# Performance work log

Measured on AMD Instinct MI355X. Metric: run time of the kernel, lower is better.

Reference implementation:

```python
import jax, jax.numpy as jnp
import numpy as np

EMBED_DIMS = 256
NUM_GROUPS = 8
NUM_LEVELS = 4
NUM_CAMS = 6
NUM_LEARNABLE_PTS = 6
FIX_SCALE = np.array([[0,0,0],[0.45,0,0],[-0.45,0,0],[0,0.45,0],[0,-0.45,0],[0,0,0.45],[0,0,-0.45]], dtype=np.float32)
NUM_PTS = len(FIX_SCALE) + NUM_LEARNABLE_PTS  # 13
GROUP_DIMS = EMBED_DIMS // NUM_GROUPS


def safe_sigmoid(x):
    return jax.nn.sigmoid(jnp.clip(x, -9.21, 9.21))


def get_rotation_matrix(q):
    # q: [..., 4] quaternion (w, x, y, z), normalized first (GaussianFormer convention)
    q = q / jnp.linalg.norm(q, axis=-1, keepdims=True)
    w, x, y, z = q[..., 0], q[..., 1], q[..., 2], q[..., 3]
    R = jnp.stack([
        jnp.stack([1 - 2 * (y * y + z * z), 2 * (x * y - w * z), 2 * (x * z + w * y)], axis=-1),
        jnp.stack([2 * (x * y + w * z), 1 - 2 * (x * x + z * z), 2 * (y * z - w * x)], axis=-1),
        jnp.stack([2 * (x * z - w * y), 2 * (y * z + w * x), 1 - 2 * (x * x + y * y)], axis=-1),
    ], axis=-2)
    return R  # [..., 3, 3]


def key_points_generator(anchor, instance_feature, W_learn, b_learn):
    bs, num_anchor = anchor.shape[:2]
    fix_scale = jnp.asarray(FIX_SCALE, anchor.dtype)  # [7, 3]
    scale = jnp.broadcast_to(fix_scale[None, None], (bs, num_anchor, fix_scale.shape[0], 3))
    learnable = safe_sigmoid((instance_feature @ W_learn + b_learn)
                             .reshape(bs, num_anchor, NUM_LEARNABLE_PTS, 3)) - 0.5
    scale = jnp.concatenate([scale, learnable], axis=-2)         # [bs, na, P, 3]
    gs_scales = anchor[..., None, 3:6]                           # [bs, na, 1, 3]
    key_points = scale * gs_scales                               # [bs, na, P, 3]
    rot_T = jnp.swapaxes(get_rotation_matrix(anchor[..., 6:10]), -1, -2)  # [bs, na, 3, 3]
    key_points = jnp.einsum('bnij,bnpj->bnpi', rot_T, key_points)
    return key_points + anchor[..., None, :3]                    # [bs, na, P, 3]


def project_points(key_points, projection_mat, image_wh):
    # key_points [bs, na, P, 3], projection_mat [bs, cams, 4, 4]
    ones = jnp.ones_like(key_points[..., :1])
    pts4 = jnp.concatenate([key_points, ones], axis=-1)          # [bs, na, P, 4]
    p2d = jnp.einsum('bcij,bnpj->bcnpi', projection_mat, pts4)   # [bs, cams, na, P, 4]
    p2d = p2d[..., :2] / jnp.maximum(p2d[..., 2:3], 1e-5)
    p2d = p2d / image_wh[:, :, None, None]
    return jnp.clip(p2d, 0.0, 0.9999)                            # [bs, cams, na, P, 2]


def bilinear_sample(feat, pts):
    # feat [bs, cams, C, H, W], pts [bs, P, cams, 2] normalized to [0,1]
    bs, cams, C, H, W = feat.shape
    x = pts[..., 0] * W - 0.5
    y = pts[..., 1] * H - 0.5
    x0 = jnp.floor(x); y0 = jnp.floor(y)
    wx = x - x0; wy = y - y0
    x0i = x0.astype(jnp.int32); y0i = y0.astype(jnp.int32)
    feat_f = jnp.transpose(feat, (0, 1, 3, 4, 2)).reshape(bs, cams, H * W, C)
    b_idx = jnp.arange(bs)[:, None, None]
    c_idx = jnp.arange(cams)[None, None, :]

    def gather(yy, xx):
        valid = (yy >= 0) & (yy < H) & (xx >= 0) & (xx < W)
        yc = jnp.clip(yy, 0, H - 1)
        xc = jnp.clip(xx, 0, W - 1)
        v = feat_f[b_idx, c_idx, yc * W + xc]                    # [bs, P, cams, C]
        return v * valid[..., None].astype(v.dtype)

    v00 = gather(y0i, x0i)
    v01 = gather(y0i, x0i + 1)
    v10 = gather(y0i + 1, x0i)
    v11 = gather(y0i + 1, x0i + 1)
    wx = wx[..., None]; wy = wy[..., None]
    return (v00 * (1 - wx) * (1 - wy) + v01 * wx * (1 - wy)
            + v10 * (1 - wx) * wy + v11 * wx * wy)               # [bs, P, cams, C]


def deformable_aggregate(feature_maps, points_2d, weights):
    # points_2d [bs, P, cams, 2]; weights [bs, P, cams, levels, groups]
    bs, P = points_2d.shape[:2]
    out = jnp.zeros((bs, P, NUM_GROUPS, GROUP_DIMS), points_2d.dtype)
    for l, feat in enumerate(feature_maps):
        samp = bilinear_sample(feat, points_2d)                  # [bs, P, cams, C]
        samp = samp.reshape(bs, P, feat.shape[1], NUM_GROUPS, GROUP_DIMS)
        out = out + jnp.einsum('bpcgd,bpcg->bpgd', samp, weights[:, :, :, l, :])
    return out.reshape(bs, P, EMBED_DIMS)


def _forward(pts3d, instance_feature, anchor, feat0, feat1, feat2, feat3,
             projection_mat, image_wh, W_learn, b_learn, W_wts, b_wts, W_out, b_out):
    bs, num_anchor = instance_feature.shape[:2]
    key_points = key_points_generator(anchor, instance_feature, W_learn, b_learn)
    # softmax weights over cams*levels*pts jointly, per group
    w = (instance_feature @ W_wts + b_wts).reshape(bs, num_anchor, -1, NUM_GROUPS)
    w = jax.nn.softmax(w, axis=-2)
    w = w.reshape(bs, num_anchor, NUM_CAMS, NUM_LEVELS, NUM_PTS, NUM_GROUPS)
    w = jnp.transpose(w, (0, 1, 4, 2, 3, 5)).reshape(bs, num_anchor * NUM_PTS, NUM_CAMS, NUM_LEVELS, NUM_GROUPS)
    p2d = project_points(key_points, projection_mat, image_wh)   # [bs, cams, na, P, 2]
    p2d = jnp.transpose(p2d, (0, 2, 3, 1, 4)).reshape(bs, num_anchor * NUM_PTS, NUM_CAMS, 2)
    feats = deformable_aggregate([feat0, feat1, feat2, feat3], p2d, w)
    feats = feats.reshape(bs, num_anchor, NUM_PTS, EMBED_DIMS).sum(axis=2)
    output = feats @ W_out + b_out
    return output + instance_feature


def setup_inputs() -> dict:
    key = jax.random.key(0)
    ks = jax.random.split(key, 16)
    bs, na = 1, 4096
    shapes = [(bs, 6, 256, 64, 176), (bs, 6, 256, 32, 88), (bs, 6, 256, 16, 44), (bs, 6, 256, 8, 22)]
    inp = {
        'pts3d': jax.random.normal(ks[0], (100000, 3), jnp.float32),
        'instance_feature': jax.random.normal(ks[1], (bs, na, EMBED_DIMS), jnp.float32),
        'anchor': jax.random.normal(ks[2], (bs, na, 11), jnp.float32),
        'feat0': jax.random.normal(ks[3], shapes[0], jnp.float32),
        'feat1': jax.random.normal(ks[4], shapes[1], jnp.float32),
        'feat2': jax.random.normal(ks[5], shapes[2], jnp.float32),
        'feat3': jax.random.normal(ks[6], shapes[3], jnp.float32),
        'projection_mat': jax.random.normal(ks[7], (bs, NUM_CAMS, 4, 4), jnp.float32),
        'image_wh': jnp.broadcast_to(jnp.array([704.0, 256.0], jnp.float32), (bs, NUM_CAMS, 2)),
        'W_learn': jax.random.normal(ks[8], (EMBED_DIMS, NUM_LEARNABLE_PTS * 3), jnp.float32) * 0.02,
        'b_learn': jnp.zeros((NUM_LEARNABLE_PTS * 3,), jnp.float32),
        'W_wts': jax.random.normal(ks[9], (EMBED_DIMS, NUM_GROUPS * NUM_CAMS * NUM_LEVELS * NUM_PTS), jnp.float32) * 0.02,
        'b_wts': jnp.zeros((NUM_GROUPS * NUM_CAMS * NUM_LEVELS * NUM_PTS,), jnp.float32),
        'W_out': jax.random.normal(ks[10], (EMBED_DIMS, EMBED_DIMS), jnp.float32) * 0.02,
        'b_out': jnp.zeros((EMBED_DIMS,), jnp.float32),
    }
    return inp


def reference(pts3d, instance_feature, anchor, feat0, feat1, feat2, feat3,
              projection_mat, image_wh, W_learn, b_learn, W_wts, b_wts, W_out, b_out):
    return _forward(pts3d, instance_feature, anchor, feat0, feat1, feat2, feat3,
                    projection_mat, image_wh, W_learn, b_learn, W_wts, b_wts, W_out, b_out)
```

## Files before the change

kernel.cpp:

```cpp
#include <hip/hip_runtime.h>
#include <math.h>


#define FT_L0 0
#define FT_L1 17301504
#define FT_L2 21626880
#define FT_L3 22708224
#define WS_LOGB 5744640
#define WS_FEATB 10856448
#define WS_LEARN 11380736
#define WS_AB 11454464
#define WS_BB 11978752
#define WS_WOB 12306432

typedef float v2f __attribute__((ext_vector_type(2)));
typedef __attribute__((ext_vector_type(8))) short bf16x8;
typedef __attribute__((ext_vector_type(4))) float f32x4;

__device__ const float FIXS[7][3] = {
    {0.f, 0.f, 0.f},  {0.45f, 0.f, 0.f}, {-0.45f, 0.f, 0.f}, {0.f, 0.45f, 0.f},
    {0.f, -0.45f, 0.f}, {0.f, 0.f, 0.45f}, {0.f, 0.f, -0.45f}};

__device__ __forceinline__ unsigned int f2bf(float f) {
  unsigned int u = __float_as_uint(f);
  u += 0x7fffu + ((u >> 16) & 1u);
  return u >> 16;
}
__device__ __forceinline__ float bf2f(unsigned short u) {
  return __uint_as_float(((unsigned int)u) << 16);
}

__global__ __launch_bounds__(256) void k_transpose_all(
    const float* __restrict__ f0, const float* __restrict__ f1,
    const float* __restrict__ f2, const float* __restrict__ f3,
    unsigned char* __restrict__ featF) {
  const int bx = blockIdx.x;
  const float* src;
  unsigned char* dst;
  int H, W, xt;
  if (bx < 6)       { src = f0; dst = featF + FT_L0; H = 64; W = 176; xt = bx * 32; }
  else if (bx < 9)  { src = f1; dst = featF + FT_L1; H = 32; W = 88;  xt = (bx - 6) * 32; }
  else if (bx < 11) { src = f2; dst = featF + FT_L2; H = 16; W = 44;  xt = (bx - 9) * 32; }
  else              { src = f3; dst = featF + FT_L3; H = 8;  W = 22;  xt = 0; }
  const int y = blockIdx.y;
  if (y >= H) return;
  __shared__ float tile[32][33];
  const int tid = threadIdx.x;
  const int i = tid & 31;
  const int j = tid >> 5;
  const int c = blockIdx.z >> 3;
  const int cht = (blockIdx.z & 7) * 32;
#pragma unroll
  for (int jj = j; jj < 32; jj += 8) {
    int x = xt + i;
    float v = 0.f;
    if (x < W) v = src[((c * 256 + cht + jj) * H + y) * W + x];
    tile[jj][i] = v;
  }
  __syncthreads();
  const int q = tid & 7;
  const int xw = tid >> 3;
  const int x = xt + xw;
  if (x < W) {
    const float v0 = tile[q * 4 + 0][xw];
    const float v1 = tile[q * 4 + 1][xw];
    const float v2 = tile[q * 4 + 2][xw];
    const float v3 = tile[q * 4 + 3][xw];
    int pk = __builtin_amdgcn_cvt_pk_fp8_f32(v0, v1, 0, false);
    pk = __builtin_amdgcn_cvt_pk_fp8_f32(v2, v3, pk, true);
    *(unsigned int*)(dst + (((c * H + y) * W + x) * 256) + cht + q * 4) =
        (unsigned int)pk;
  }
}

__global__ __launch_bounds__(256) void k_prep_pack(
    const float* __restrict__ iw, const float* __restrict__ Ww,
    const float* __restrict__ Wl, const float* __restrict__ Wo,
    unsigned short* __restrict__ Ab, unsigned short* __restrict__ Bb,
    unsigned short* __restrict__ Wob) {
  __shared__ unsigned short tile[32][33];
  const int tid = threadIdx.x;
  const int bx = blockIdx.x;
  if (bx < 1024) {
    const int i = bx * 256 + tid;
    const float4 v = ((const float4*)iw)[i];
    uint2 o;
    o.x = f2bf(v.x) | (f2bf(v.y) << 16);
    o.y = f2bf(v.z) | (f2bf(v.w) << 16);
    ((uint2*)Ab)[i] = o;
    return;
  }
  const int i = tid & 31;
  const int r = tid >> 5;
  if (bx < 1664) {
    const int idx = bx - 1024;
    const int j0 = (idx % 80) * 32;
    const int k0 = (idx / 80) * 32;
#pragma unroll
    for (int rr = r; rr < 32; rr += 8) {
      const int k = k0 + rr, j = j0 + i;
      float v = 0.f;
      if (j < 2496) v = Ww[k * 2496 + j];
      else if (j < 2514) v = Wl[k * 18 + (j - 2496)];
      tile[rr][i] = (unsigned short)f2bf(v);
    }
    __syncthreads();
#pragma unroll
    for (int rr = r; rr < 32; rr += 8)
      Bb[(j0 + rr) * 256 + k0 + i] = tile[i][rr];
  } else {
    const int idx = bx - 1664;
    const int j0 = (idx & 7) * 32;
    const int k0 = (idx >> 3) * 32;
#pragma unroll
    for (int rr = r; rr < 32; rr += 8)
      tile[rr][i] = (unsigned short)f2bf(Wo[(k0 + rr) * 256 + j0 + i]);
    __syncthreads();
#pragma unroll
    for (int rr = r; rr < 32; rr += 8)
      Wob[(j0 + rr) * 256 + k0 + i] = tile[i][rr];
  }
}

__global__ __launch_bounds__(256) void k_wts_mfma(
    const unsigned short* __restrict__ Ab, const unsigned short* __restrict__ Bb,
    const float* __restrict__ b_wts, const float* __restrict__ b_learn,
    unsigned short* __restrict__ logitsB, float* __restrict__ learn) {
  const int tid = threadIdx.x;
  const int w = tid >> 6, lane = tid & 63;
  const int ml = lane & 15, q = lane >> 4;
  const int n0 = blockIdx.x * 64;
  const int m0 = blockIdx.y * 64;
  f32x4 acc[4] = {{0.f, 0.f, 0.f, 0.f}, {0.f, 0.f, 0.f, 0.f},
                  {0.f, 0.f, 0.f, 0.f}, {0.f, 0.f, 0.f, 0.f}};
  const unsigned short* Ap = Ab + (m0 + w * 16 + ml) * 256 + q * 8;
  const unsigned short* Bp = Bb + (n0 + ml) * 256 + q * 8;
#pragma unroll
  for (int kk = 0; kk < 8; ++kk) {
    const bf16x8 a = *(const bf16x8*)(Ap + kk * 32);
#pragma unroll
    for (int nt = 0; nt < 4; ++nt) {
      const bf16x8 b = *(const bf16x8*)(Bp + nt * 16 * 256 + kk * 32);
      acc[nt] = __builtin_amdgcn_mfma_f32_16x16x32_bf16(a, b, acc[nt], 0, 0, 0);
    }
  }
  const int rowb = m0 + w * 16 + q * 4;
#pragma unroll
  for (int nt = 0; nt < 4; ++nt) {
    const int col = n0 + nt * 16 + ml;
    if (col < 2496) {
      const float b = b_wts[col];
#pragma unroll
      for (int r = 0; r < 4; ++r)
        logitsB[(rowb + r) * 2496 + col] = (unsigned short)f2bf(acc[nt][r] + b);
    } else if (col < 2514) {
      const float b = b_learn[col - 2496];
#pragma unroll
      for (int r = 0; r < 4; ++r) {
        float v = fminf(fmaxf(acc[nt][r] + b, -9.21f), 9.21f);
        learn[(rowb + r) * 18 + (col - 2496)] = 1.f / (1.f + expf(-v)) - 0.5f;
      }
    }
  }
}

__global__ __launch_bounds__(256, 6) void k_sample(
    const float* __restrict__ anchor, const unsigned short* __restrict__ logitsB,
    const float* __restrict__ learn_g, const unsigned char* __restrict__ featF,
    const float* __restrict__ proj, const float* __restrict__ wh,
    unsigned short* __restrict__ featsB) {
  const int n = blockIdx.x;
  const int tid = threadIdx.x;
  const int lane = tid & 63;
  const int wave = tid >> 6;
  __shared__ unsigned short s_w[8 * 328];
  __shared__ float s_p2d[78][2];
  __shared__ float s_learn[18];
  __shared__ int4 s_off[320];
  __shared__ float4 s_wt[320];
  __shared__ float s_red[4][256];

  for (int i = tid; i < 2496; i += 256) {
    const int s = i >> 3, g = i & 7;
    const int c = s / 52;
    const int r = s - c * 52;
    const int l = r / 13;
    const int p = r - l * 13;
    s_w[g * 328 + (p * 6 + c) * 4 + l] = logitsB[n * 2496 + i];
  }
  if (tid < 64) s_w[(tid >> 3) * 328 + 312 + (tid & 7)] = 0;
  if (tid < 18) s_learn[tid] = learn_g[n * 18 + tid];
  __syncthreads();

#pragma unroll
  for (int gg = 0; gg < 2; ++gg) {
    unsigned short* row = &s_w[(wave * 2 + gg) * 328];
    float l[5];
    float mx = -1e30f;
#pragma unroll
    for (int i = 0; i < 5; ++i) {
      const int s = lane + i * 64;
      l[i] = (s < 312) ? bf2f(row[s]) : -1e30f;
      mx = fmaxf(mx, l[i]);
    }
    for (int off = 32; off; off >>= 1) mx = fmaxf(mx, __shfl_xor(mx, off));
    float sum = 0.f;
#pragma unroll
    for (int i = 0; i < 5; ++i) {
      l[i] = __expf(l[i] - mx);
      sum += l[i];
    }
    for (int off = 32; off; off >>= 1) sum += __shfl_xor(sum, off);
    const float inv = 1.f / sum;
#pragma unroll
    for (int i = 0; i < 5; ++i) {
      const int s = lane + i * 64;
      if (s < 312) row[s] = (unsigned short)f2bf(l[i] * inv);
    }
  }

  if (tid < 78) {
    const int p = tid / 6, c = tid % 6;
    const float* an = anchor + n * 11;
    float qw = an[6], qx = an[7], qy = an[8], qz = an[9];
    const float qinv = 1.f / sqrtf(qw * qw + qx * qx + qy * qy + qz * qz);
    qw *= qinv; qx *= qinv; qy *= qinv; qz *= qinv;
    const float R00 = 1.f - 2.f * (qy * qy + qz * qz), R01 = 2.f * (qx * qy - qw * qz), R02 = 2.f * (qx * qz + qw * qy);
    const float R10 = 2.f * (qx * qy + qw * qz), R11 = 1.f - 2.f * (qx * qx + qz * qz), R12 = 2.f * (qy * qz - qw * qx);
    const float R20 = 2.f * (qx * qz - qw * qy), R21 = 2.f * (qy * qz + qw * qx), R22 = 1.f - 2.f * (qx * qx + qy * qy);
    float s0, s1, s2;
    if (p < 7) {
      s0 = FIXS[p][0]; s1 = FIXS[p][1]; s2 = FIXS[p][2];
    } else {
      const int b = (p - 7) * 3;
      s0 = s_learn[b]; s1 = s_learn[b + 1]; s2 = s_learn[b + 2];
    }
    const float vx = s0 * an[3], vy = s1 * an[4], vz = s2 * an[5];
    const float kx = R00 * vx + R10 * vy + R20 * vz + an[0];
    const float ky = R01 * vx + R11 * vy + R21 * vz + an[1];
    const float kz = R02 * vx + R12 * vy + R22 * vz + an[2];
    const float* P = proj + c * 16;
    const float h0 = P[0] * kx + P[1] * ky + P[2] * kz + P[3];
    const float h1 = P[4] * kx + P[5] * ky + P[6] * kz + P[7];
    const float h2 = P[8] * kx + P[9] * ky + P[10] * kz + P[11];
    const float zz = fmaxf(h2, 1e-5f);
    float px = h0 / zz / wh[c * 2 + 0];
    float py = h1 / zz / wh[c * 2 + 1];
    px = fminf(fmaxf(px, 0.f), 0.9999f);
    py = fminf(fmaxf(py, 0.f), 0.9999f);
    s_p2d[tid][0] = px;
    s_p2d[tid][1] = py;
  }
  __syncthreads();

  {
    constexpr int LBB[4] = {FT_L0, FT_L1, FT_L2, FT_L3};
    constexpr int CSB[4] = {2883584, 720896, 180224, 45056};
    for (int t = tid; t < 320; t += 256) {
      const int pc = t >> 2, l = t & 3;
      if (pc >= 78) {
        s_off[t] = make_int4(0, 0, 0, 0);
        s_wt[t] = make_float4(0.f, 0.f, 0.f, 0.f);
        continue;
      }
      const int c = pc % 6;
      const int H = 64 >> l, W = 176 >> l;
      const float fx = s_p2d[pc][0] * (float)W - 0.5f;
      const float fy = s_p2d[pc][1] * (float)H - 0.5f;
      const float x0f = floorf(fx), y0f = floorf(fy);
      const float wx = fx - x0f, wy = fy - y0f;
      const int x0 = (int)x0f, y0 = (int)y0f;
      const float mx0 = (x0 >= 0) ? 1.f : 0.f;
      const float mx1 = (x0 + 1 < W) ? 1.f : 0.f;
      const float my0 = (y0 >= 0) ? 1.f : 0.f;
      const float my1 = (y0 + 1 < H) ? 1.f : 0.f;
      const int cx0 = max(x0, 0), cx1 = min(x0 + 1, W - 1);
      const int cy0 = max(y0, 0), cy1 = min(y0 + 1, H - 1);
      const int base = LBB[l] + c * CSB[l];
      int4 o;
      o.x = base + (cy0 * W + cx0) * 256;
      o.y = base + (cy0 * W + cx1) * 256;
      o.z = base + (cy1 * W + cx0) * 256;
      o.w = base + (cy1 * W + cx1) * 256;
      s_off[t] = o;
      float4 w4;
      w4.x = (1.f - wx) * (1.f - wy) * mx0 * my0;
      w4.y = wx * (1.f - wy) * mx1 * my0;
      w4.z = (1.f - wx) * wy * mx0 * my1;
      w4.w = wx * wy * mx1 * my1;
      s_wt[t] = w4;
    }
  }
  __syncthreads();

  const int q = lane >> 4;
  const int ql = lane & 15;
  const int chb = ql * 16;
  const int g = ql >> 1;
  v2f acc[8];
#pragma unroll
  for (int k = 0; k < 8; ++k) acc[k] = (v2f){0.f, 0.f};
  const unsigned char* fb = featF;
  const unsigned short* wrow = &s_w[g * 328];
  const int pcb = wave * 4 + q;
#pragma unroll
  for (int it = 0; it < 5; ++it) {
    const int pc = pcb + it * 16;
    const int t0 = pc * 4;
    const uint2 wq = *(const uint2*)&wrow[t0];
    float wgl[4];
    wgl[0] = __uint_as_float(wq.x << 16);
    wgl[1] = __uint_as_float(wq.x & 0xffff0000u);
    wgl[2] = __uint_as_float(wq.y << 16);
    wgl[3] = __uint_as_float(wq.y & 0xffff0000u);
#pragma unroll
    for (int l4 = 0; l4 < 4; ++l4) {
      const int t = t0 + l4;
      const int4 o = s_off[t];
      const float4 bw = s_wt[t];
      const float wg = wgl[l4];
      const uint4 u0 = *(const uint4*)(fb + (o.x + chb));
      const uint4 u1 = *(const uint4*)(fb + (o.y + chb));
      const uint4 u2 = *(const uint4*)(fb + (o.z + chb));
      const uint4 u3 = *(const uint4*)(fb + (o.w + chb));
      const float s0 = bw.x * wg, s1 = bw.y * wg, s2 = bw.z * wg, s3 = bw.w * wg;
      const v2f w0 = {s0, s0}, w1 = {s1, s1}, w2 = {s2, s2}, w3 = {s3, s3};
      acc[0] += __builtin_amdgcn_cvt_pk_f32_fp8((int)u0.x, false) * w0;
      acc[1] += __builtin_amdgcn_cvt_pk_f32_fp8((int)u0.x, true)  * w0;
      acc[2] += __builtin_amdgcn_cvt_pk_f32_fp8((int)u0.y, false) * w0;
      acc[3] += __builtin_amdgcn_cvt_pk_f32_fp8((int)u0.y, true)  * w0;
      acc[4] += __builtin_amdgcn_cvt_pk_f32_fp8((int)u0.z, false) * w0;
      acc[5] += __builtin_amdgcn_cvt_pk_f32_fp8((int)u0.z, true)  * w0;
      acc[6] += __builtin_amdgcn_cvt_pk_f32_fp8((int)u0.w, false) * w0;
      acc[7] += __builtin_amdgcn_cvt_pk_f32_fp8((int)u0.w, true)  * w0;
      acc[0] += __builtin_amdgcn_cvt_pk_f32_fp8((int)u1.x, false) * w1;
      acc[1] += __builtin_amdgcn_cvt_pk_f32_fp8((int)u1.x, true)  * w1;
      acc[2] += __builtin_amdgcn_cvt_pk_f32_fp8((int)u1.y, false) * w1;
      acc[3] += __builtin_amdgcn_cvt_pk_f32_fp8((int)u1.y, true)  * w1;
      acc[4] += __builtin_amdgcn_cvt_pk_f32_fp8((int)u1.z, false) * w1;
      acc[5] += __builtin_amdgcn_cvt_pk_f32_fp8((int)u1.z, true)  * w1;
      acc[6] += __builtin_amdgcn_cvt_pk_f32_fp8((int)u1.w, false) * w1;
      acc[7] += __builtin_amdgcn_cvt_pk_f32_fp8((int)u1.w, true)  * w1;
      acc[0] += __builtin_amdgcn_cvt_pk_f32_fp8((int)u2.x, false) * w2;
      acc[1] += __builtin_amdgcn_cvt_pk_f32_fp8((int)u2.x, true)  * w2;
      acc[2] += __builtin_amdgcn_cvt_pk_f32_fp8((int)u2.y, false) * w2;
      acc[3] += __builtin_amdgcn_cvt_pk_f32_fp8((int)u2.y, true)  * w2;
      acc[4] += __builtin_amdgcn_cvt_pk_f32_fp8((int)u2.z, false) * w2;
      acc[5] += __builtin_amdgcn_cvt_pk_f32_fp8((int)u2.z, true)  * w2;
      acc[6] += __builtin_amdgcn_cvt_pk_f32_fp8((int)u2.w, false) * w2;
      acc[7] += __builtin_amdgcn_cvt_pk_f32_fp8((int)u2.w, true)  * w2;
      acc[0] += __builtin_amdgcn_cvt_pk_f32_fp8((int)u3.x, false) * w3;
      acc[1] += __builtin_amdgcn_cvt_pk_f32_fp8((int)u3.x, true)  * w3;
      acc[2] += __builtin_amdgcn_cvt_pk_f32_fp8((int)u3.y, false) * w3;
      acc[3] += __builtin_amdgcn_cvt_pk_f32_fp8((int)u3.y, true)  * w3;
      acc[4] += __builtin_amdgcn_cvt_pk_f32_fp8((int)u3.z, false) * w3;
      acc[5] += __builtin_amdgcn_cvt_pk_f32_fp8((int)u3.z, true)  * w3;
      acc[6] += __builtin_amdgcn_cvt_pk_f32_fp8((int)u3.w, false) * w3;
      acc[7] += __builtin_amdgcn_cvt_pk_f32_fp8((int)u3.w, true)  * w3;
    }
  }
#pragma unroll
  for (int k = 0; k < 8; ++k) {
    v2f b;
    b.x = __shfl_xor(acc[k].x, 16);
    b.y = __shfl_xor(acc[k].y, 16);
    acc[k] += b;
    b.x = __shfl_xor(acc[k].x, 32);
    b.y = __shfl_xor(acc[k].y, 32);
    acc[k] += b;
  }
  if (lane < 16) {
    float* dst = &s_red[wave][ql * 16];
    *(float4*)(dst + 0)  = make_float4(acc[0].x, acc[0].y, acc[1].x, acc[1].y);
    *(float4*)(dst + 4)  = make_float4(acc[2].x, acc[2].y, acc[3].x, acc[3].y);
    *(float4*)(dst + 8)  = make_float4(acc[4].x, acc[4].y, acc[5].x, acc[5].y);
    *(float4*)(dst + 12) = make_float4(acc[6].x, acc[6].y, acc[7].x, acc[7].y);
  }
  __syncthreads();
  {
    const float sum = s_red[0][tid] + s_red[1][tid] + s_red[2][tid] + s_red[3][tid];
    featsB[n * 256 + tid] = (unsigned short)f2bf(sum);
  }
}

__global__ __launch_bounds__(256) void k_out_mfma(
    const unsigned short* __restrict__ Ab, const unsigned short* __restrict__ Bb,
    const float* __restrict__ bias, const float* __restrict__ resid,
    float* __restrict__ out) {
  const int tid = threadIdx.x;
  const int w = tid >> 6, lane = tid & 63;
  const int ml = lane & 15, q = lane >> 4;
  const int n0 = blockIdx.x * 64;
  const int m0 = blockIdx.y * 64;
  f32x4 acc[4] = {{0.f, 0.f, 0.f, 0.f}, {0.f, 0.f, 0.f, 0.f},
                  {0.f, 0.f, 0.f, 0.f}, {0.f, 0.f, 0.f, 0.f}};
  const unsigned short* Ap = Ab + (m0 + w * 16 + ml) * 256 + q * 8;
  const unsigned short* Bp = Bb + (n0 + ml) * 256 + q * 8;
#pragma unroll
  for (int kk = 0; kk < 8; ++kk) {
    const bf16x8 a = *(const bf16x8*)(Ap + kk * 32);
#pragma unroll
    for (int nt = 0; nt < 4; ++nt) {
      const bf16x8 b = *(const bf16x8*)(Bp + nt * 16 * 256 + kk * 32);
      acc[nt] = __builtin_amdgcn_mfma_f32_16x16x32_bf16(a, b, acc[nt], 0, 0, 0);
    }
  }
  const int rowb = m0 + w * 16 + q * 4;
#pragma unroll
  for (int nt = 0; nt < 4; ++nt) {
    const int col = n0 + nt * 16 + ml;
    const float b = bias[col];
#pragma unroll
    for (int r = 0; r < 4; ++r) {
      const int row = rowb + r;
      out[row * 256 + col] = acc[nt][r] + b + resid[row * 256 + col];
    }
  }
}

extern "C" void kernel_launch(void* const* d_in, const int* in_sizes, int n_in,
                              void* d_out, int out_size, void* d_ws, size_t ws_size,
                              hipStream_t stream) {
  (void)in_sizes; (void)n_in; (void)out_size; (void)ws_size;
  const float* iw      = (const float*)d_in[1];
  const float* anchor  = (const float*)d_in[2];
  const float* f0      = (const float*)d_in[3];
  const float* f1      = (const float*)d_in[4];
  const float* f2      = (const float*)d_in[5];
  const float* f3      = (const float*)d_in[6];
  const float* proj    = (const float*)d_in[7];
  const float* wh      = (const float*)d_in[8];
  const float* W_learn = (const float*)d_in[9];
  const float* b_learn = (const float*)d_in[10];
  const float* W_wts   = (const float*)d_in[11];
  const float* b_wts   = (const float*)d_in[12];
  const float* W_out   = (const float*)d_in[13];
  const float* b_out   = (const float*)d_in[14];
  float* out = (float*)d_out;
  float* ws = (float*)d_ws;
  unsigned char*  featF   = (unsigned char*)ws;
  unsigned short* logitsB = (unsigned short*)(ws + WS_LOGB);
  unsigned short* featsB  = (unsigned short*)(ws + WS_FEATB);
  float*          learn   = ws + WS_LEARN;
  unsigned short* Ab      = (unsigned short*)(ws + WS_AB);
  unsigned short* Bb      = (unsigned short*)(ws + WS_BB);
  unsigned short* Wob     = (unsigned short*)(ws + WS_WOB);

  k_transpose_all<<<dim3(12, 64, 48), 256, 0, stream>>>(f0, f1, f2, f3, featF);
  k_prep_pack<<<1728, 256, 0, stream>>>(iw, W_wts, W_learn, W_out, Ab, Bb, Wob);
  k_wts_mfma<<<dim3(40, 64), 256, 0, stream>>>(Ab, Bb, b_wts, b_learn, logitsB, learn);
  k_sample<<<4096, 256, 0, stream>>>(anchor, logitsB, learn, featF, proj, wh, featsB);
  k_out_mfma<<<dim3(4, 64), 256, 0, stream>>>(featsB, Wob, b_out, iw, out);
}
```

Baseline: 303.9 us.

## Permute weight columns and fuse exp into GEMM epilogue to simplify softmax load

The weight matrix columns are reordered during packing so the GEMM writes logits already in the per-group padded layout that the sampling kernel uses. The exp is applied in the GEMM epilogue, so the sampling kernel loads with a plain contiguous copy and only sums and normalizes. The max-subtraction is dropped, which relies on the logits staying small enough not to overflow, and the sampling kernel's launch bounds are raised to 8 blocks per SM. The GEMM grows slightly because of the padded columns.

```diff
diff --git a/kernel.cpp b/kernel.cpp
--- a/kernel.cpp
+++ b/kernel.cpp
@@ -6,12 +6,13 @@
 #define FT_L1 17301504
 #define FT_L2 21626880
 #define FT_L3 22708224
-#define WS_LOGB 5744640
-#define WS_FEATB 10856448
-#define WS_LEARN 11380736
-#define WS_AB 11454464
-#define WS_BB 11978752
-#define WS_WOB 12306432
+#define WS_LOGE 5744640
+#define WS_FEATB 11118592
+#define WS_LEARN 11642880
+#define WS_AB 11716608
+#define WS_BB 12240896
+#define WS_WOB 12584960
+#define WS_BIASP 12617728
 
 typedef float v2f __attribute__((ext_vector_type(2)));
 typedef __attribute__((ext_vector_type(8))) short bf16x8;
@@ -73,11 +74,28 @@
   }
 }
 
+__device__ __forceinline__ int rowmap(int rp, int* srcj) {
+  if (rp < 2624) {
+    const int g = rp / 328;
+    const int u = rp - g * 328;
+    if (u < 312) {
+      const int pc = u >> 2, l = u & 3;
+      const int p = pc / 6, c = pc - p * 6;
+      *srcj = (c * 52 + l * 13 + p) * 8 + g;
+      return 0;
+    }
+    return 2;
+  }
+  if (rp < 2642) { *srcj = rp - 2624; return 1; }
+  return 2;
+}
+
 __global__ __launch_bounds__(256) void k_prep_pack(
     const float* __restrict__ iw, const float* __restrict__ Ww,
     const float* __restrict__ Wl, const float* __restrict__ Wo,
+    const float* __restrict__ bw, const float* __restrict__ bl,
     unsigned short* __restrict__ Ab, unsigned short* __restrict__ Bb,
-    unsigned short* __restrict__ Wob) {
+    unsigned short* __restrict__ Wob, float* __restrict__ biasP) {
   __shared__ unsigned short tile[32][33];
   const int tid = threadIdx.x;
   const int bx = blockIdx.x;
@@ -92,24 +110,26 @@
   }
   const int i = tid & 31;
   const int r = tid >> 5;
-  if (bx < 1664) {
+  if (bx < 1696) {
     const int idx = bx - 1024;
-    const int j0 = (idx % 80) * 32;
-    const int k0 = (idx / 80) * 32;
+    const int j0 = (idx % 84) * 32;
+    const int k0 = (idx / 84) * 32;
+    int srcj = 0;
+    const int mode = rowmap(j0 + i, &srcj);
 #pragma unroll
     for (int rr = r; rr < 32; rr += 8) {
-      const int k = k0 + rr, j = j0 + i;
+      const int k = k0 + rr;
       float v = 0.f;
-      if (j < 2496) v = Ww[k * 2496 + j];
-      else if (j < 2514) v = Wl[k * 18 + (j - 2496)];
+      if (mode == 0) v = Ww[k * 2496 + srcj];
+      else if (mode == 1) v = Wl[k * 18 + srcj];
       tile[rr][i] = (unsigned short)f2bf(v);
     }
     __syncthreads();
 #pragma unroll
     for (int rr = r; rr < 32; rr += 8)
       Bb[(j0 + rr) * 256 + k0 + i] = tile[i][rr];
-  } else {
-    const int idx = bx - 1664;
+  } else if (bx < 1760) {
+    const int idx = bx - 1696;
     const int j0 = (idx & 7) * 32;
     const int k0 = (idx >> 3) * 32;
 #pragma unroll
@@ -119,13 +139,23 @@
 #pragma unroll
     for (int rr = r; rr < 32; rr += 8)
       Wob[(j0 + rr) * 256 + k0 + i] = tile[i][rr];
+  } else {
+    const int rp = (bx - 1760) * 256 + tid;
+    if (rp < 2688) {
+      int srcj = 0;
+      const int mode = rowmap(rp, &srcj);
+      float b = 0.f;
+      if (mode == 0) b = bw[(srcj >> 3)];
+      else if (mode == 1) b = bl[srcj];
+      biasP[rp] = b;
+    }
   }
 }
 
 __global__ __launch_bounds__(256) void k_wts_mfma(
     const unsigned short* __restrict__ Ab, const unsigned short* __restrict__ Bb,
-    const float* __restrict__ b_wts, const float* __restrict__ b_learn,
-    unsigned short* __restrict__ logitsB, float* __restrict__ learn) {
+    const float* __restrict__ biasP,
+    unsigned short* __restrict__ logitsE, float* __restrict__ learn) {
   const int tid = threadIdx.x;
   const int w = tid >> 6, lane = tid & 63;
   const int ml = lane & 15, q = lane >> 4;
@@ -148,24 +178,23 @@
 #pragma unroll
   for (int nt = 0; nt < 4; ++nt) {
     const int col = n0 + nt * 16 + ml;
-    if (col < 2496) {
-      const float b = b_wts[col];
+    const float b = biasP[col];
+    if (col < 2624) {
 #pragma unroll
       for (int r = 0; r < 4; ++r)
-        logitsB[(rowb + r) * 2496 + col] = (unsigned short)f2bf(acc[nt][r] + b);
-    } else if (col < 2514) {
-      const float b = b_learn[col - 2496];
+        logitsE[(rowb + r) * 2624 + col] = (unsigned short)f2bf(__expf(acc[nt][r] + b));
+    } else if (col < 2642) {
 #pragma unroll
       for (int r = 0; r < 4; ++r) {
         float v = fminf(fmaxf(acc[nt][r] + b, -9.21f), 9.21f);
-        learn[(rowb + r) * 18 + (col - 2496)] = 1.f / (1.f + expf(-v)) - 0.5f;
+        learn[(rowb + r) * 18 + (col - 2624)] = 1.f / (1.f + expf(-v)) - 0.5f;
       }
     }
   }
 }
 
-__global__ __launch_bounds__(256, 6) void k_sample(
-    const float* __restrict__ anchor, const unsigned short* __restrict__ logitsB,
+__global__ __launch_bounds__(256, 8) void k_sample(
+    const float* __restrict__ anchor, const unsigned short* __restrict__ logitsE,
     const float* __restrict__ learn_g, const unsigned char* __restrict__ featF,
     const float* __restrict__ proj, const float* __restrict__ wh,
     unsigned short* __restrict__ featsB) {
@@ -180,15 +209,11 @@
   __shared__ float4 s_wt[320];
   __shared__ float s_red[4][256];
 
-  for (int i = tid; i < 2496; i += 256) {
-    const int s = i >> 3, g = i & 7;
-    const int c = s / 52;
-    const int r = s - c * 52;
-    const int l = r / 13;
-    const int p = r - l * 13;
-    s_w[g * 328 + (p * 6 + c) * 4 + l] = logitsB[n * 2496 + i];
-  }
-  if (tid < 64) s_w[(tid >> 3) * 328 + 312 + (tid & 7)] = 0;
+  {
+    const unsigned int* src = (const unsigned int*)(logitsE + n * 2624);
+    unsigned int* dstw = (unsigned int*)s_w;
+    for (int i = tid; i < 1312; i += 256) dstw[i] = src[i];
+  }
   if (tid < 18) s_learn[tid] = learn_g[n * 18 + tid];
   __syncthreads();
 
@@ -196,18 +221,11 @@
   for (int gg = 0; gg < 2; ++gg) {
     unsigned short* row = &s_w[(wave * 2 + gg) * 328];
     float l[5];
-    float mx = -1e30f;
+    float sum = 0.f;
 #pragma unroll
     for (int i = 0; i < 5; ++i) {
       const int s = lane + i * 64;
-      l[i] = (s < 312) ? bf2f(row[s]) : -1e30f;
-      mx = fmaxf(mx, l[i]);
-    }
-    for (int off = 32; off; off >>= 1) mx = fmaxf(mx, __shfl_xor(mx, off));
-    float sum = 0.f;
-#pragma unroll
-    for (int i = 0; i < 5; ++i) {
-      l[i] = __expf(l[i] - mx);
+      l[i] = (s < 312) ? bf2f(row[s]) : 0.f;
       sum += l[i];
     }
     for (int off = 32; off; off >>= 1) sum += __shfl_xor(sum, off);
@@ -439,16 +457,18 @@
   float* out = (float*)d_out;
   float* ws = (float*)d_ws;
   unsigned char*  featF   = (unsigned char*)ws;
-  unsigned short* logitsB = (unsigned short*)(ws + WS_LOGB);
+  unsigned short* logitsE = (unsigned short*)(ws + WS_LOGE);
   unsigned short* featsB  = (unsigned short*)(ws + WS_FEATB);
   float*          learn   = ws + WS_LEARN;
   unsigned short* Ab      = (unsigned short*)(ws + WS_AB);
   unsigned short* Bb      = (unsigned short*)(ws + WS_BB);
   unsigned short* Wob     = (unsigned short*)(ws + WS_WOB);
+  float*          biasP   = ws + WS_BIASP;
 
   k_transpose_all<<<dim3(12, 64, 48), 256, 0, stream>>>(f0, f1, f2, f3, featF);
-  k_prep_pack<<<1728, 256, 0, stream>>>(iw, W_wts, W_learn, W_out, Ab, Bb, Wob);
-  k_wts_mfma<<<dim3(40, 64), 256, 0, stream>>>(Ab, Bb, b_wts, b_learn, logitsB, learn);
-  k_sample<<<4096, 256, 0, stream>>>(anchor, logitsB, learn, featF, proj, wh, featsB);
+  k_prep_pack<<<1771, 256, 0, stream>>>(iw, W_wts, W_learn, W_out, b_wts, b_learn,
+                                        Ab, Bb, Wob, biasP);
+  k_wts_mfma<<<dim3(42, 64), 256, 0, stream>>>(Ab, Bb, biasP, logitsE, learn);
+  k_sample<<<4096, 256, 0, stream>>>(anchor, logitsE, learn, featF, proj, wh, featsB);
   k_out_mfma<<<dim3(4, 64), 256, 0, stream>>>(featsB, Wob, b_out, iw, out);
 }
```

Result: no change. 303.9 us (+0.0%).
